# Kernel tuning notes

Hardware: AMD Instinct MI355X
Metric: run time of the kernel (lower is better)

Reference implementation:

```python
import jax, jax.numpy as jnp
import numpy as np
from functools import partial

B, S, H = 1, 2048, 1024
F, E, K = 2048, 8, 2


def setup_inputs() -> dict:
    key = jax.random.key(0)
    ks = jax.random.split(key, 7)
    x = jax.random.normal(ks[0], (B, S, H), dtype=jnp.float32)
    weights = jax.random.uniform(ks[1], (B * S, E), dtype=jnp.float32)
    top_weights = jax.random.uniform(ks[2], (B * S, K), dtype=jnp.float32)
    top_experts = jax.random.randint(ks[3], (B * S, K), 0, E).astype(jnp.int64)
    scale = 0.02  # keep activations in a sane range
    w1 = jax.random.normal(ks[4], (E, F, H), dtype=jnp.float32) * scale
    v1 = jax.random.normal(ks[5], (E, F, H), dtype=jnp.float32) * scale
    w2 = jax.random.normal(ks[6], (E, F, H), dtype=jnp.float32) * scale
    return {"x": x, "weights": weights, "top_weights": top_weights,
            "top_experts": top_experts, "w1": w1, "v1": v1, "w2": w2}


def _moe_forward(x, top_weights, top_experts, w1, v1, w2):
    b, s, h = x.shape
    xf = x.reshape(-1, h)  # [T, H]
    n_exp = w1.shape[0]
    # combine weight per (token, expert): sum over top-k slots routed to e
    onehot = jax.nn.one_hot(top_experts, n_exp, dtype=x.dtype)      # [T, K, E]
    cw = jnp.einsum('tk,tke->et', top_weights, onehot)              # [E, T]

    def body(acc, inputs):
        w1e, v1e, w2e, cwe = inputs  # [F,H], [F,H], [F,H], [T]
        gate = jax.nn.silu(xf @ w1e.T)       # [T, F]
        inter = gate * (xf @ v1e.T)          # GLU
        down = inter @ w2e                   # [T, H]
        return acc + cwe[:, None] * down, None

    out, _ = jax.lax.scan(body, jnp.zeros_like(xf), (w1, v1, w2, cw))
    return out.reshape(b, s, h)


def reference(x, weights, top_weights, top_experts, w1, v1, w2):
    # `weights` (full router probs) is accepted but unused, as in the original.
    return _moe_forward(x, top_weights, top_experts, w1, v1, w2)
```

## Files before the change

kernel.cpp:

```cpp
#include <hip/hip_runtime.h>
#include <hip/hip_bf16.h>


#define T_ 2048
#define H_ 1024
#define F_ 2048
#define E_ 8

#define SCAP 768
#define MAXT2 (E_ * SCAP / 128)

typedef unsigned short u16;
typedef short s8v __attribute__((ext_vector_type(8)));
typedef float f4v __attribute__((ext_vector_type(4)));
typedef unsigned short u16x4 __attribute__((ext_vector_type(4)));

__device__ __forceinline__ u16 f2bf(float f) {
    union { float f; unsigned u; } v; v.f = f;
    unsigned r = v.u + 0x7FFF + ((v.u >> 16) & 1);
    return (u16)(r >> 16);
}
__device__ __forceinline__ unsigned pkbf(float a, float b) {
    __hip_bfloat162 h = __float22bfloat162_rn(make_float2(a, b));
    union { __hip_bfloat162 h; unsigned u; } c; c.h = h; return c.u;
}
__device__ __forceinline__ int4 cvt8(const float4 a, const float4 b) {
    int4 r; r.x = (int)pkbf(a.x, a.y); r.y = (int)pkbf(a.z, a.w);
    r.z = (int)pkbf(b.x, b.y); r.w = (int)pkbf(b.z, b.w); return r;
}
__device__ __forceinline__ void async16(void* lds, const void* g) {
    __builtin_amdgcn_global_load_lds(
        (const __attribute__((address_space(1))) unsigned*)g,
        (__attribute__((address_space(3))) unsigned*)lds, 16, 0, 0);
}

__global__ void router_kernel(const int* __restrict__ te, const float* __restrict__ tw,
                              int* __restrict__ slot_tok, float* __restrict__ slot_w,
                              int* __restrict__ tile_e, int* __restrict__ tile_s,
                              int* __restrict__ ntiles) {
    __shared__ int cnt[E_];
    __shared__ int s_any;
    int tid = threadIdx.x;
    if (tid < E_) cnt[tid] = 0;
    if (tid == 0) s_any = 0;
    __syncthreads();
    int any = 0;
    for (int i = tid; i < 2 * T_; i += 256) if (i & 1) any |= te[i];
    if (any) atomicOr(&s_any, 1);
    __syncthreads();
    bool is32 = (s_any != 0);
    for (int t = tid; t < T_; t += 256) {
        int e0 = is32 ? te[2 * t]     : te[4 * t];
        int e1 = is32 ? te[2 * t + 1] : te[4 * t + 2];
        float w0 = tw[2 * t], w1 = tw[2 * t + 1];
        if (e0 == e1) {
            int p = atomicAdd(&cnt[e0], 1);
            if (p < SCAP) { slot_tok[e0 * SCAP + p] = t; slot_w[e0 * SCAP + p] = w0 + w1; }
        } else {
            int p = atomicAdd(&cnt[e0], 1);
            if (p < SCAP) { slot_tok[e0 * SCAP + p] = t; slot_w[e0 * SCAP + p] = w0; }
            p = atomicAdd(&cnt[e1], 1);
            if (p < SCAP) { slot_tok[e1 * SCAP + p] = t; slot_w[e1 * SCAP + p] = w1; }
        }
    }
    __syncthreads();
    for (int e = 0; e < E_; ++e) {
        int c = min(cnt[e], SCAP);
        int pc = min((c + 127) & ~127, SCAP);
        for (int p = c + tid; p < pc; p += 256) {
            slot_tok[e * SCAP + p] = -1; slot_w[e * SCAP + p] = 0.f;
        }
    }
    __syncthreads();
    if (tid == 0) {
        int nt = 0;
        for (int e = 0; e < E_; ++e) {
            int pc = min((min(cnt[e], SCAP) + 127) & ~127, SCAP);
            for (int s = 0; s < pc; s += 128) { tile_e[nt] = e; tile_s[nt] = e * SCAP + s; ++nt; }
        }
        *ntiles = nt;
    }
}

__global__ void cvt_kernel(const float* __restrict__ src, u16* __restrict__ dst) {
    int i = (blockIdx.x * 256 + threadIdx.x) * 4;
    float4 v = *(const float4*)(src + i);
    u16x4 o = { f2bf(v.x), f2bf(v.y), f2bf(v.z), f2bf(v.w) };
    *(u16x4*)(dst + i) = o;
}

__global__ void tcvt8_kernel(const float* __restrict__ src0, u16* __restrict__ dst0) {
    const float* src = src0 + (size_t)blockIdx.z * F_ * H_;
    u16* dst = dst0 + (size_t)blockIdx.z * H_ * F_;
    __shared__ __align__(16) u16 tile[64][72];
    int bc = blockIdx.x * 64, br = blockIdx.y * 64;
    int tx = threadIdx.x, ty = threadIdx.y;
    for (int r = ty; r < 64; r += 32) {
        const float* p = src + (size_t)(br + r) * H_ + bc + tx * 8;
        float4 v0 = *(const float4*)p;
        float4 v1 = *(const float4*)(p + 4);
        u16* q = &tile[r][tx * 8];
        q[0] = f2bf(v0.x); q[1] = f2bf(v0.y); q[2] = f2bf(v0.z); q[3] = f2bf(v0.w);
        q[4] = f2bf(v1.x); q[5] = f2bf(v1.y); q[6] = f2bf(v1.z); q[7] = f2bf(v1.w);
    }
    __syncthreads();
    for (int c = ty; c < 64; c += 32) {
        u16 tmp[8];
#pragma unroll
        for (int j = 0; j < 8; ++j) tmp[j] = tile[tx * 8 + j][c];
        *(int4*)&dst[(size_t)(bc + c) * F_ + br + tx * 8] = *(int4*)tmp;
    }
}

__global__ void gather_x_kernel(const float* __restrict__ x, const int* __restrict__ slot_tok,
                                const int* __restrict__ tile_s, const int* __restrict__ ntiles,
                                u16* __restrict__ xg) {
    if ((int)blockIdx.x >= *ntiles) return;
    int base = tile_s[blockIdx.x];
    int tid = threadIdx.x;
    __shared__ int stok[128];
    if (tid < 128) stok[tid] = slot_tok[base + tid];
    __syncthreads();
    for (int c = tid; c < 128 * 128; c += 256) {
        int r = c >> 7, co = (c & 127) * 8;
        int tok = stok[r];
        u16* dst = xg + ((size_t)(base + r) << 10) + co;
        if (tok < 0) { *(int4*)dst = make_int4(0, 0, 0, 0); }
        else {
            const float* p = x + ((size_t)tok << 10) + co;
            *(int4*)dst = cvt8(*(const float4*)p, *(const float4*)(p + 4));
        }
    }
}

__global__ __launch_bounds__(256, 2) void glu_async_kernel(
        const u16* __restrict__ xg, const u16* __restrict__ w1b,
        const u16* __restrict__ v1b, const int* __restrict__ tile_e,
        const int* __restrict__ tile_s, const int* __restrict__ ntiles,
        const float* __restrict__ slot_w, u16* __restrict__ inter) {
    int bt = blockIdx.y;
    if (bt >= *ntiles) return;
    int e = tile_e[bt], s0 = tile_s[bt];
    int f0 = blockIdx.x * 128;
    __shared__ __align__(16) u16 As[128 * 32];
    __shared__ __align__(16) u16 B1s[128 * 32];
    __shared__ __align__(16) u16 B2s[128 * 32];
    __shared__ float swv[128];
    int tid = threadIdx.x;
    int lane = tid & 63, wave = tid >> 6;
    int wm = wave >> 1, wn = wave & 1;
    int ml = lane & 15, q = lane >> 4;
    if (tid < 128) swv[tid] = slot_w[s0 + tid];

    int acol = (lane & 3) << 3;
    int row0 = (wave << 4) + (lane >> 2);
    int row1 = row0 + 64;
    const u16* gA0  = xg + ((size_t)(s0 + row0) << 10) + acol;
    const u16* gA1  = xg + ((size_t)(s0 + row1) << 10) + acol;
    const size_t wofs = (size_t)e * F_ * H_;
    const u16* gB10 = w1b + wofs + ((size_t)(f0 + row0) << 10) + acol;
    const u16* gB11 = w1b + wofs + ((size_t)(f0 + row1) << 10) + acol;
    const u16* gB20 = v1b + wofs + ((size_t)(f0 + row0) << 10) + acol;
    const u16* gB21 = v1b + wofs + ((size_t)(f0 + row1) << 10) + acol;
    u16* lA0  = As  + (row0 << 5) + acol;
    u16* lA1  = As  + (row1 << 5) + acol;
    u16* lB10 = B1s + (row0 << 5) + acol;
    u16* lB11 = B1s + (row1 << 5) + acol;
    u16* lB20 = B2s + (row0 << 5) + acol;
    u16* lB21 = B2s + (row1 << 5) + acol;

    f4v accg[4][4] = {};
    f4v accu[4][4] = {};

    for (int k0 = 0; k0 < H_; k0 += 32) {
        __syncthreads();
        async16(lA0,  gA0  + k0);
        async16(lA1,  gA1  + k0);
        async16(lB10, gB10 + k0);
        async16(lB11, gB11 + k0);
        async16(lB20, gB20 + k0);
        async16(lB21, gB21 + k0);
        __syncthreads();
        s8v a[4], b1[4], b2[4];
#pragma unroll
        for (int i = 0; i < 4; ++i) {
            a[i]  = *(const s8v*)(As  + (wm * 64 + i * 16 + ml) * 32 + q * 8);
            b1[i] = *(const s8v*)(B1s + (wn * 64 + i * 16 + ml) * 32 + q * 8);
            b2[i] = *(const s8v*)(B2s + (wn * 64 + i * 16 + ml) * 32 + q * 8);
        }
#pragma unroll
        for (int i = 0; i < 4; ++i)
#pragma unroll
            for (int j = 0; j < 4; ++j) {
                accg[i][j] = __builtin_amdgcn_mfma_f32_16x16x32_bf16(a[i], b1[j], accg[i][j], 0, 0, 0);
                accu[i][j] = __builtin_amdgcn_mfma_f32_16x16x32_bf16(a[i], b2[j], accu[i][j], 0, 0, 0);
            }
    }
#pragma unroll
    for (int i = 0; i < 4; ++i)
#pragma unroll
        for (int r = 0; r < 4; ++r) {
            int lr = wm * 64 + i * 16 + q * 4 + r;
            float cv = swv[lr];
#pragma unroll
            for (int j = 0; j < 4; ++j) {
                float g = accg[i][j][r];
                float u = accu[i][j][r];
                float s = g / (1.f + __expf(-g));
                int f = f0 + wn * 64 + j * 16 + ml;
                inter[((size_t)(s0 + lr) << 11) + f] = f2bf(cv * s * u);
            }
        }
}

__global__ __launch_bounds__(256, 2) void down_async_kernel(
        const u16* __restrict__ inter, const u16* __restrict__ w2bT,
        const int* __restrict__ tile_e, const int* __restrict__ tile_s,
        const int* __restrict__ ntiles, const int* __restrict__ slot_tok,
        float* __restrict__ out) {
    int bt = blockIdx.y;
    if (bt >= *ntiles) return;
    int e = tile_e[bt], s0 = tile_s[bt];
    int h0 = blockIdx.x * 128;
    int kbeg = blockIdx.z * (F_ / 2);
    __shared__ __align__(16) u16 As[128 * 32];
    __shared__ __align__(16) u16 Bs[128 * 32];
    __shared__ int stok[128];
    int tid = threadIdx.x;
    int lane = tid & 63, wave = tid >> 6;
    int wm = wave >> 1, wn = wave & 1;
    int ml = lane & 15, q = lane >> 4;
    if (tid < 128) stok[tid] = slot_tok[s0 + tid];

    int acol = (lane & 3) << 3;
    int row0 = (wave << 4) + (lane >> 2);
    int row1 = row0 + 64;
    const u16* gA0 = inter + ((size_t)(s0 + row0) << 11) + kbeg + acol;
    const u16* gA1 = inter + ((size_t)(s0 + row1) << 11) + kbeg + acol;
    const u16* gB0 = w2bT + (size_t)e * H_ * F_ + ((size_t)(h0 + row0) << 11) + kbeg + acol;
    const u16* gB1 = w2bT + (size_t)e * H_ * F_ + ((size_t)(h0 + row1) << 11) + kbeg + acol;
    u16* lA0 = As + (row0 << 5) + acol;
    u16* lA1 = As + (row1 << 5) + acol;
    u16* lB0 = Bs + (row0 << 5) + acol;
    u16* lB1 = Bs + (row1 << 5) + acol;

    f4v acc[4][4] = {};
    for (int k0 = 0; k0 < F_ / 2; k0 += 32) {
        __syncthreads();
        async16(lA0, gA0 + k0);
        async16(lA1, gA1 + k0);
        async16(lB0, gB0 + k0);
        async16(lB1, gB1 + k0);
        __syncthreads();
        s8v a[4], b[4];
#pragma unroll
        for (int i = 0; i < 4; ++i) {
            a[i] = *(const s8v*)(As + (wm * 64 + i * 16 + ml) * 32 + q * 8);
            b[i] = *(const s8v*)(Bs + (wn * 64 + i * 16 + ml) * 32 + q * 8);
        }
#pragma unroll
        for (int i = 0; i < 4; ++i)
#pragma unroll
            for (int j = 0; j < 4; ++j)
                acc[i][j] = __builtin_amdgcn_mfma_f32_16x16x32_bf16(a[i], b[j], acc[i][j], 0, 0, 0);
    }
#pragma unroll
    for (int i = 0; i < 4; ++i)
#pragma unroll
        for (int r = 0; r < 4; ++r) {
            int lr = wm * 64 + i * 16 + q * 4 + r;
            int tok = stok[lr];
            if (tok < 0) continue;
            size_t trow = (size_t)tok << 10;
#pragma unroll
            for (int j = 0; j < 4; ++j) {
                int h = h0 + wn * 64 + j * 16 + ml;
                atomicAdd(&out[trow + h], acc[i][j][r]);
            }
        }
}

#define SCAP3 1024
__global__ void router3_kernel(const int* __restrict__ te, const float* __restrict__ tw,
                               int* __restrict__ cnt_g, int* __restrict__ slot_tok,
                               float* __restrict__ slot_w) {
    __shared__ int cnt[E_];
    __shared__ int s_any;
    int tid = threadIdx.x;
    if (tid < E_) cnt[tid] = 0;
    if (tid == 0) s_any = 0;
    __syncthreads();
    int any = 0;
    for (int i = tid; i < 2 * T_; i += 256) if (i & 1) any |= te[i];
    if (any) atomicOr(&s_any, 1);
    __syncthreads();
    bool is32 = (s_any != 0);
    for (int t = tid; t < T_; t += 256) {
        int e0 = is32 ? te[2 * t]     : te[4 * t];
        int e1 = is32 ? te[2 * t + 1] : te[4 * t + 2];
        float w0 = tw[2 * t], w1 = tw[2 * t + 1];
        if (e0 == e1) {
            int p = atomicAdd(&cnt[e0], 1);
            if (p < SCAP3) { slot_tok[e0 * SCAP3 + p] = t; slot_w[e0 * SCAP3 + p] = w0 + w1; }
        } else {
            int p = atomicAdd(&cnt[e0], 1);
            if (p < SCAP3) { slot_tok[e0 * SCAP3 + p] = t; slot_w[e0 * SCAP3 + p] = w0; }
            p = atomicAdd(&cnt[e1], 1);
            if (p < SCAP3) { slot_tok[e1 * SCAP3 + p] = t; slot_w[e1 * SCAP3 + p] = w1; }
        }
    }
    __syncthreads();
    for (int e = 0; e < E_; ++e) {
        int c = min(cnt[e], SCAP3);
        int pc = min((c + 127) & ~127, SCAP3);
        for (int p = c + tid; p < pc; p += 256) {
            slot_tok[e * SCAP3 + p] = 0; slot_w[e * SCAP3 + p] = 0.f;
        }
    }
    if (tid < E_) cnt_g[tid] = min(cnt[tid], SCAP3);
}
__global__ __launch_bounds__(256, 2) void glu3_kernel(
        const u16* __restrict__ xb, const float* __restrict__ w1,
        const float* __restrict__ v1, const int* __restrict__ cnt_g,
        const int* __restrict__ slot_tok, const float* __restrict__ slot_w,
        u16* __restrict__ inter) {
    int e = blockIdx.x >> 3, tt = blockIdx.x & 7;
    if (tt * 128 >= cnt_g[e]) return;
    __shared__ __align__(16) u16 As[128 * 32];
    __shared__ __align__(16) u16 B1s[128 * 32];
    __shared__ __align__(16) u16 B2s[128 * 32];
    __shared__ int stok[128];
    __shared__ float sw[128];
    int tid = threadIdx.x;
    if (tid < 128) {
        stok[tid] = slot_tok[e * SCAP3 + tt * 128 + tid];
        sw[tid]   = slot_w[e * SCAP3 + tt * 128 + tid];
    }
    __syncthreads();
    int lane = tid & 63, wave = tid >> 6;
    int wm = wave >> 1, wn = wave & 1;
    int f0 = blockIdx.y * 128;
    int ml = lane & 15, q = lane >> 4;
    int r0 = tid >> 2, r1 = 64 + (tid >> 2);
    int colo = (tid & 3) * 8;
    const size_t tokoff0 = (size_t)stok[r0] * H_ + colo;
    const size_t tokoff1 = (size_t)stok[r1] * H_ + colo;
    const float* gb1 = w1 + (size_t)e * F_ * H_ + (size_t)f0 * H_;
    const float* gb2 = v1 + (size_t)e * F_ * H_ + (size_t)f0 * H_;
    const size_t boff0 = (size_t)r0 * H_ + colo;
    const size_t boff1 = (size_t)r1 * H_ + colo;
    f4v accg[4][4] = {};
    f4v accu[4][4] = {};
    for (int k0 = 0; k0 < H_; k0 += 32) {
        __syncthreads();
        *(int4*)(As + tid * 8)         = *(const int4*)(xb + tokoff0 + k0);
        *(int4*)(As + (256 + tid) * 8) = *(const int4*)(xb + tokoff1 + k0);
        const float* p = gb1 + boff0 + k0;
        *(int4*)(B1s + tid * 8) = cvt8(*(const float4*)p, *(const float4*)(p + 4));
        p = gb1 + boff1 + k0;
        *(int4*)(B1s + (256 + tid) * 8) = cvt8(*(const float4*)p, *(const float4*)(p + 4));
        p = gb2 + boff0 + k0;
        *(int4*)(B2s + tid * 8) = cvt8(*(const float4*)p, *(const float4*)(p + 4));
        p = gb2 + boff1 + k0;
        *(int4*)(B2s + (256 + tid) * 8) = cvt8(*(const float4*)p, *(const float4*)(p + 4));
        __syncthreads();
        s8v a[4], b1[4], b2[4];
#pragma unroll
        for (int i = 0; i < 4; ++i) {
            a[i]  = *(const s8v*)(As  + (wm * 64 + i * 16 + ml) * 32 + q * 8);
            b1[i] = *(const s8v*)(B1s + (wn * 64 + i * 16 + ml) * 32 + q * 8);
            b2[i] = *(const s8v*)(B2s + (wn * 64 + i * 16 + ml) * 32 + q * 8);
        }
#pragma unroll
        for (int i = 0; i < 4; ++i)
#pragma unroll
            for (int j = 0; j < 4; ++j) {
                accg[i][j] = __builtin_amdgcn_mfma_f32_16x16x32_bf16(a[i], b1[j], accg[i][j], 0, 0, 0);
                accu[i][j] = __builtin_amdgcn_mfma_f32_16x16x32_bf16(a[i], b2[j], accu[i][j], 0, 0, 0);
            }
    }
#pragma unroll
    for (int i = 0; i < 4; ++i)
#pragma unroll
        for (int r = 0; r < 4; ++r) {
            int lr = wm * 64 + i * 16 + q * 4 + r;
            float cv = sw[lr];
#pragma unroll
            for (int j = 0; j < 4; ++j) {
                float g = accg[i][j][r];
                float u = accu[i][j][r];
                float s = g / (1.f + __expf(-g));
                int f = f0 + wn * 64 + j * 16 + ml;
                inter[(size_t)(e * SCAP3 + tt * 128 + lr) * F_ + f] = f2bf(cv * s * u);
            }
        }
}
__global__ __launch_bounds__(256) void down3_kernel(
        const u16* __restrict__ inter, const u16* __restrict__ w2bT,
        const int* __restrict__ cnt_g, const int* __restrict__ slot_tok,
        float* __restrict__ out) {
    int e = blockIdx.x >> 3, tt = blockIdx.x & 7;
    if (tt * 128 >= cnt_g[e]) return;
    __shared__ __align__(16) u16 As[128 * 32];
    __shared__ __align__(16) u16 Bs[128 * 32];
    __shared__ int stok[128];
    int tid = threadIdx.x;
    if (tid < 128) stok[tid] = slot_tok[e * SCAP3 + tt * 128 + tid];
    __syncthreads();
    int lane = tid & 63, wave = tid >> 6;
    int wm = wave >> 1, wn = wave & 1;
    int h0 = blockIdx.y * 128;
    int ml = lane & 15, q = lane >> 4;
    int kbeg = blockIdx.z * (F_ / 2), kend = kbeg + (F_ / 2);
    f4v acc[4][4] = {};
    const u16* ga = inter + (size_t)(e * SCAP3 + tt * 128) * F_;
    const u16* gb = w2bT + (size_t)e * H_ * F_ + (size_t)h0 * F_;
    for (int k0 = kbeg; k0 < kend; k0 += 32) {
        __syncthreads();
#pragma unroll
        for (int p = 0; p < 2; ++p) {
            int c = p * 256 + tid;
            int r = c >> 2, co = (c & 3) * 8;
            *(int4*)(As + c * 8) = *(const int4*)(ga + (size_t)r * F_ + k0 + co);
            *(int4*)(Bs + c * 8) = *(const int4*)(gb + (size_t)r * F_ + k0 + co);
        }
        __syncthreads();
        s8v a[4], b[4];
#pragma unroll
        for (int i = 0; i < 4; ++i) {
            a[i] = *(const s8v*)(As + (wm * 64 + i * 16 + ml) * 32 + q * 8);
            b[i] = *(const s8v*)(Bs + (wn * 64 + i * 16 + ml) * 32 + q * 8);
        }
#pragma unroll
        for (int i = 0; i < 4; ++i)
#pragma unroll
            for (int j = 0; j < 4; ++j)
                acc[i][j] = __builtin_amdgcn_mfma_f32_16x16x32_bf16(a[i], b[j], acc[i][j], 0, 0, 0);
    }
#pragma unroll
    for (int i = 0; i < 4; ++i)
#pragma unroll
        for (int r = 0; r < 4; ++r) {
            int lr = wm * 64 + i * 16 + q * 4 + r;
            size_t trow = (size_t)stok[lr] * H_;
#pragma unroll
            for (int j = 0; j < 4; ++j) {
                int h = h0 + wn * 64 + j * 16 + ml;
                atomicAdd(&out[trow + h], acc[i][j][r]);
            }
        }
}

extern "C" void kernel_launch(void* const* d_in, const int* in_sizes, int n_in,
                              void* d_out, int out_size, void* d_ws, size_t ws_size,
                              hipStream_t stream) {
    const float* x  = (const float*)d_in[0];
    const float* tw = (const float*)d_in[2];
    const int*   te = (const int*)d_in[3];
    const float* w1 = (const float*)d_in[4];
    const float* v1 = (const float*)d_in[5];
    const float* w2 = (const float*)d_in[6];
    float* out = (float*)d_out;
    char* ws = (char*)d_ws;

    if (ws_size >= ((size_t)135 << 20)) {
        int*   tile_e   = (int*)(ws + (1 << 10));
        int*   tile_s   = (int*)(ws + (2 << 10));
        int*   ntiles   = (int*)(ws + 256);
        int*   slot_tok = (int*)(ws + (4 << 10));
        float* slot_w   = (float*)(ws + (32 << 10));
        u16*   xg       = (u16*)(ws + ((size_t)1 << 20));
        u16*   w1b      = (u16*)(ws + ((size_t)13 << 20));
        u16*   v1b      = (u16*)(ws + ((size_t)45 << 20));
        u16*   w2bT     = (u16*)(ws + ((size_t)77 << 20));
        u16*   inter    = (u16*)(ws + ((size_t)109 << 20));

        hipMemsetAsync(out, 0, (size_t)T_ * H_ * sizeof(float), stream);
        router_kernel<<<1, 256, 0, stream>>>(te, tw, slot_tok, slot_w, tile_e, tile_s, ntiles);
        cvt_kernel<<<(E_ * F_ * H_) / 1024, 256, 0, stream>>>(w1, w1b);
        cvt_kernel<<<(E_ * F_ * H_) / 1024, 256, 0, stream>>>(v1, v1b);
        tcvt8_kernel<<<dim3(H_ / 64, F_ / 64, E_), dim3(8, 32), 0, stream>>>(w2, w2bT);
        gather_x_kernel<<<MAXT2, 256, 0, stream>>>(x, slot_tok, tile_s, ntiles, xg);
        glu_async_kernel<<<dim3(F_ / 128, MAXT2), 256, 0, stream>>>(
            xg, w1b, v1b, tile_e, tile_s, ntiles, slot_w, inter);
        down_async_kernel<<<dim3(H_ / 128, MAXT2, 2), 256, 0, stream>>>(
            inter, w2bT, tile_e, tile_s, ntiles, slot_tok, out);
    } else {
        int*   cnt_g    = (int*)(ws);
        int*   slot_tok = (int*)(ws + (4 << 10));
        float* slot_w   = (float*)(ws + (64 << 10));
        u16*   xb       = (u16*)(ws + ((size_t)1 << 20));
        u16*   w2bT     = (u16*)(ws + ((size_t)5 << 20));
        u16*   inter    = (u16*)(ws + ((size_t)37 << 20));

        hipMemsetAsync(out, 0, (size_t)T_ * H_ * sizeof(float), stream);
        router3_kernel<<<1, 256, 0, stream>>>(te, tw, cnt_g, slot_tok, slot_w);
        cvt_kernel<<<(T_ * H_) / 1024, 256, 0, stream>>>(x, xb);
        tcvt8_kernel<<<dim3(H_ / 64, F_ / 64, E_), dim3(8, 32), 0, stream>>>(w2, w2bT);
        glu3_kernel<<<dim3(E_ * 8, F_ / 128), 256, 0, stream>>>(
            xb, w1, v1, cnt_g, slot_tok, slot_w, inter);
        down3_kernel<<<dim3(E_ * 8, H_ / 128, 2), 256, 0, stream>>>(
            inter, w2bT, cnt_g, slot_tok, out);
    }
}
```

Before: 374.3 us.

## Halve GEMM N-tiles, replace atomic scatter with per-slot buffers and combine kernel

Shrinks the N tile of both grouped GEMMs from 128 to 64 and raises the occupancy hint, doubling block count to fill more CUs. The down-projection now writes plain stores into two split-K per-slot buffers (reusing the w1b/v1b workspace once they are consumed), and a new combine kernel gathers each token's two slots, removing the output memset and fp32 atomics. The router also records a token-to-slot map, and the w1/v1 conversions are merged into one launch. In exchange each A tile is reloaded twice as often, and the extra buffer write plus read and one more kernel launch add traffic.

```diff
diff --git a/kernel.cpp b/kernel.cpp
--- a/kernel.cpp
+++ b/kernel.cpp
@@ -8,7 +8,8 @@
 #define E_ 8
 
 #define SCAP 768
-#define MAXT2 (E_ * SCAP / 128)
+#define NSLOT (E_ * SCAP)
+#define MAXT2 (NSLOT / 128)
 
 typedef unsigned short u16;
 typedef short s8v __attribute__((ext_vector_type(8)));
@@ -36,6 +37,7 @@
 
 __global__ void router_kernel(const int* __restrict__ te, const float* __restrict__ tw,
                               int* __restrict__ slot_tok, float* __restrict__ slot_w,
+                              int* __restrict__ tok_slot,
                               int* __restrict__ tile_e, int* __restrict__ tile_s,
                               int* __restrict__ ntiles) {
     __shared__ int cnt[E_];
@@ -55,12 +57,18 @@
         float w0 = tw[2 * t], w1 = tw[2 * t + 1];
         if (e0 == e1) {
             int p = atomicAdd(&cnt[e0], 1);
-            if (p < SCAP) { slot_tok[e0 * SCAP + p] = t; slot_w[e0 * SCAP + p] = w0 + w1; }
+            int s = (p < SCAP) ? e0 * SCAP + p : -1;
+            if (s >= 0) { slot_tok[s] = t; slot_w[s] = w0 + w1; }
+            tok_slot[2 * t] = s; tok_slot[2 * t + 1] = -1;
         } else {
             int p = atomicAdd(&cnt[e0], 1);
-            if (p < SCAP) { slot_tok[e0 * SCAP + p] = t; slot_w[e0 * SCAP + p] = w0; }
+            int s = (p < SCAP) ? e0 * SCAP + p : -1;
+            if (s >= 0) { slot_tok[s] = t; slot_w[s] = w0; }
+            tok_slot[2 * t] = s;
             p = atomicAdd(&cnt[e1], 1);
-            if (p < SCAP) { slot_tok[e1 * SCAP + p] = t; slot_w[e1 * SCAP + p] = w1; }
+            s = (p < SCAP) ? e1 * SCAP + p : -1;
+            if (s >= 0) { slot_tok[s] = t; slot_w[s] = w1; }
+            tok_slot[2 * t + 1] = s;
         }
     }
     __syncthreads();
@@ -82,7 +90,10 @@
     }
 }
 
-__global__ void cvt_kernel(const float* __restrict__ src, u16* __restrict__ dst) {
+__global__ void cvtwv_kernel(const float* __restrict__ w1, const float* __restrict__ v1,
+                             u16* __restrict__ w1b, u16* __restrict__ v1b) {
+    const float* src = blockIdx.y ? v1 : w1;
+    u16* dst = blockIdx.y ? v1b : w1b;
     int i = (blockIdx.x * 256 + threadIdx.x) * 4;
     float4 v = *(const float4*)(src + i);
     u16x4 o = { f2bf(v.x), f2bf(v.y), f2bf(v.z), f2bf(v.w) };
@@ -133,7 +144,7 @@
     }
 }
 
-__global__ __launch_bounds__(256, 2) void glu_async_kernel(
+__global__ __launch_bounds__(256, 4) void glu_async_kernel(
         const u16* __restrict__ xg, const u16* __restrict__ w1b,
         const u16* __restrict__ v1b, const int* __restrict__ tile_e,
         const int* __restrict__ tile_s, const int* __restrict__ ntiles,
@@ -141,10 +152,10 @@
     int bt = blockIdx.y;
     if (bt >= *ntiles) return;
     int e = tile_e[bt], s0 = tile_s[bt];
-    int f0 = blockIdx.x * 128;
+    int f0 = blockIdx.x * 64;
     __shared__ __align__(16) u16 As[128 * 32];
-    __shared__ __align__(16) u16 B1s[128 * 32];
-    __shared__ __align__(16) u16 B2s[128 * 32];
+    __shared__ __align__(16) u16 B1s[64 * 32];
+    __shared__ __align__(16) u16 B2s[64 * 32];
     __shared__ float swv[128];
     int tid = threadIdx.x;
     int lane = tid & 63, wave = tid >> 6;
@@ -158,40 +169,36 @@
     const u16* gA0  = xg + ((size_t)(s0 + row0) << 10) + acol;
     const u16* gA1  = xg + ((size_t)(s0 + row1) << 10) + acol;
     const size_t wofs = (size_t)e * F_ * H_;
-    const u16* gB10 = w1b + wofs + ((size_t)(f0 + row0) << 10) + acol;
-    const u16* gB11 = w1b + wofs + ((size_t)(f0 + row1) << 10) + acol;
-    const u16* gB20 = v1b + wofs + ((size_t)(f0 + row0) << 10) + acol;
-    const u16* gB21 = v1b + wofs + ((size_t)(f0 + row1) << 10) + acol;
-    u16* lA0  = As  + (row0 << 5) + acol;
-    u16* lA1  = As  + (row1 << 5) + acol;
-    u16* lB10 = B1s + (row0 << 5) + acol;
-    u16* lB11 = B1s + (row1 << 5) + acol;
-    u16* lB20 = B2s + (row0 << 5) + acol;
-    u16* lB21 = B2s + (row1 << 5) + acol;
-
-    f4v accg[4][4] = {};
-    f4v accu[4][4] = {};
+    const u16* gB1 = w1b + wofs + ((size_t)(f0 + row0) << 10) + acol;
+    const u16* gB2 = v1b + wofs + ((size_t)(f0 + row0) << 10) + acol;
+    u16* lA0 = As  + (row0 << 5) + acol;
+    u16* lA1 = As  + (row1 << 5) + acol;
+    u16* lB1 = B1s + (row0 << 5) + acol;
+    u16* lB2 = B2s + (row0 << 5) + acol;
+
+    f4v accg[4][2] = {};
+    f4v accu[4][2] = {};
 
     for (int k0 = 0; k0 < H_; k0 += 32) {
         __syncthreads();
-        async16(lA0,  gA0  + k0);
-        async16(lA1,  gA1  + k0);
-        async16(lB10, gB10 + k0);
-        async16(lB11, gB11 + k0);
-        async16(lB20, gB20 + k0);
-        async16(lB21, gB21 + k0);
-        __syncthreads();
-        s8v a[4], b1[4], b2[4];
-#pragma unroll
-        for (int i = 0; i < 4; ++i) {
+        async16(lA0, gA0 + k0);
+        async16(lA1, gA1 + k0);
+        async16(lB1, gB1 + k0);
+        async16(lB2, gB2 + k0);
+        __syncthreads();
+        s8v a[4], b1[2], b2[2];
+#pragma unroll
+        for (int i = 0; i < 4; ++i)
             a[i]  = *(const s8v*)(As  + (wm * 64 + i * 16 + ml) * 32 + q * 8);
-            b1[i] = *(const s8v*)(B1s + (wn * 64 + i * 16 + ml) * 32 + q * 8);
-            b2[i] = *(const s8v*)(B2s + (wn * 64 + i * 16 + ml) * 32 + q * 8);
+#pragma unroll
+        for (int j = 0; j < 2; ++j) {
+            b1[j] = *(const s8v*)(B1s + (wn * 32 + j * 16 + ml) * 32 + q * 8);
+            b2[j] = *(const s8v*)(B2s + (wn * 32 + j * 16 + ml) * 32 + q * 8);
         }
 #pragma unroll
         for (int i = 0; i < 4; ++i)
 #pragma unroll
-            for (int j = 0; j < 4; ++j) {
+            for (int j = 0; j < 2; ++j) {
                 accg[i][j] = __builtin_amdgcn_mfma_f32_16x16x32_bf16(a[i], b1[j], accg[i][j], 0, 0, 0);
                 accu[i][j] = __builtin_amdgcn_mfma_f32_16x16x32_bf16(a[i], b2[j], accu[i][j], 0, 0, 0);
             }
@@ -203,65 +210,63 @@
             int lr = wm * 64 + i * 16 + q * 4 + r;
             float cv = swv[lr];
 #pragma unroll
-            for (int j = 0; j < 4; ++j) {
+            for (int j = 0; j < 2; ++j) {
                 float g = accg[i][j][r];
                 float u = accu[i][j][r];
                 float s = g / (1.f + __expf(-g));
-                int f = f0 + wn * 64 + j * 16 + ml;
+                int f = f0 + wn * 32 + j * 16 + ml;
                 inter[((size_t)(s0 + lr) << 11) + f] = f2bf(cv * s * u);
             }
         }
 }
 
-__global__ __launch_bounds__(256, 2) void down_async_kernel(
+__global__ __launch_bounds__(256, 4) void down_async_kernel(
         const u16* __restrict__ inter, const u16* __restrict__ w2bT,
         const int* __restrict__ tile_e, const int* __restrict__ tile_s,
-        const int* __restrict__ ntiles, const int* __restrict__ slot_tok,
-        float* __restrict__ out) {
+        const int* __restrict__ ntiles,
+        float* __restrict__ dbufA, float* __restrict__ dbufB) {
     int bt = blockIdx.y;
     if (bt >= *ntiles) return;
     int e = tile_e[bt], s0 = tile_s[bt];
-    int h0 = blockIdx.x * 128;
-    int kbeg = blockIdx.z * (F_ / 2);
+    int h0 = blockIdx.x * 64;
+    int ks = blockIdx.z;
+    int kbeg = ks * (F_ / 2);
+    float* dbuf = ks ? dbufB : dbufA;
     __shared__ __align__(16) u16 As[128 * 32];
-    __shared__ __align__(16) u16 Bs[128 * 32];
-    __shared__ int stok[128];
+    __shared__ __align__(16) u16 Bs[64 * 32];
     int tid = threadIdx.x;
     int lane = tid & 63, wave = tid >> 6;
     int wm = wave >> 1, wn = wave & 1;
     int ml = lane & 15, q = lane >> 4;
-    if (tid < 128) stok[tid] = slot_tok[s0 + tid];
 
     int acol = (lane & 3) << 3;
     int row0 = (wave << 4) + (lane >> 2);
     int row1 = row0 + 64;
     const u16* gA0 = inter + ((size_t)(s0 + row0) << 11) + kbeg + acol;
     const u16* gA1 = inter + ((size_t)(s0 + row1) << 11) + kbeg + acol;
-    const u16* gB0 = w2bT + (size_t)e * H_ * F_ + ((size_t)(h0 + row0) << 11) + kbeg + acol;
-    const u16* gB1 = w2bT + (size_t)e * H_ * F_ + ((size_t)(h0 + row1) << 11) + kbeg + acol;
+    const u16* gB  = w2bT + (size_t)e * H_ * F_ + ((size_t)(h0 + row0) << 11) + kbeg + acol;
     u16* lA0 = As + (row0 << 5) + acol;
     u16* lA1 = As + (row1 << 5) + acol;
-    u16* lB0 = Bs + (row0 << 5) + acol;
-    u16* lB1 = Bs + (row1 << 5) + acol;
-
-    f4v acc[4][4] = {};
+    u16* lB  = Bs + (row0 << 5) + acol;
+
+    f4v acc[4][2] = {};
     for (int k0 = 0; k0 < F_ / 2; k0 += 32) {
         __syncthreads();
         async16(lA0, gA0 + k0);
         async16(lA1, gA1 + k0);
-        async16(lB0, gB0 + k0);
-        async16(lB1, gB1 + k0);
-        __syncthreads();
-        s8v a[4], b[4];
-#pragma unroll
-        for (int i = 0; i < 4; ++i) {
+        async16(lB,  gB  + k0);
+        __syncthreads();
+        s8v a[4], b[2];
+#pragma unroll
+        for (int i = 0; i < 4; ++i)
             a[i] = *(const s8v*)(As + (wm * 64 + i * 16 + ml) * 32 + q * 8);
-            b[i] = *(const s8v*)(Bs + (wn * 64 + i * 16 + ml) * 32 + q * 8);
-        }
+#pragma unroll
+        for (int j = 0; j < 2; ++j)
+            b[j] = *(const s8v*)(Bs + (wn * 32 + j * 16 + ml) * 32 + q * 8);
 #pragma unroll
         for (int i = 0; i < 4; ++i)
 #pragma unroll
-            for (int j = 0; j < 4; ++j)
+            for (int j = 0; j < 2; ++j)
                 acc[i][j] = __builtin_amdgcn_mfma_f32_16x16x32_bf16(a[i], b[j], acc[i][j], 0, 0, 0);
     }
 #pragma unroll
@@ -269,15 +274,32 @@
 #pragma unroll
         for (int r = 0; r < 4; ++r) {
             int lr = wm * 64 + i * 16 + q * 4 + r;
-            int tok = stok[lr];
-            if (tok < 0) continue;
-            size_t trow = (size_t)tok << 10;
-#pragma unroll
-            for (int j = 0; j < 4; ++j) {
-                int h = h0 + wn * 64 + j * 16 + ml;
-                atomicAdd(&out[trow + h], acc[i][j][r]);
+            float* drow = dbuf + ((size_t)(s0 + lr) << 10);
+#pragma unroll
+            for (int j = 0; j < 2; ++j) {
+                int h = h0 + wn * 32 + j * 16 + ml;
+                drow[h] = acc[i][j][r];
             }
         }
+}
+
+__global__ void combine_kernel(const float* __restrict__ dbufA, const float* __restrict__ dbufB,
+                               const int* __restrict__ tok_slot, float* __restrict__ out) {
+    int t = blockIdx.x;
+    int c = threadIdx.x * 4;
+    int s0 = tok_slot[2 * t], s1 = tok_slot[2 * t + 1];
+    float4 acc = make_float4(0.f, 0.f, 0.f, 0.f);
+    if (s0 >= 0) {
+        float4 a = *(const float4*)(dbufA + ((size_t)s0 << 10) + c);
+        float4 b = *(const float4*)(dbufB + ((size_t)s0 << 10) + c);
+        acc.x = a.x + b.x; acc.y = a.y + b.y; acc.z = a.z + b.z; acc.w = a.w + b.w;
+    }
+    if (s1 >= 0) {
+        float4 a = *(const float4*)(dbufA + ((size_t)s1 << 10) + c);
+        float4 b = *(const float4*)(dbufB + ((size_t)s1 << 10) + c);
+        acc.x += a.x + b.x; acc.y += a.y + b.y; acc.z += a.z + b.z; acc.w += a.w + b.w;
+    }
+    *(float4*)(out + ((size_t)t << 10) + c) = acc;
 }
 
 #define SCAP3 1024
@@ -318,6 +340,12 @@
         }
     }
     if (tid < E_) cnt_g[tid] = min(cnt[tid], SCAP3);
+}
+__global__ void cvt_kernel(const float* __restrict__ src, u16* __restrict__ dst) {
+    int i = (blockIdx.x * 256 + threadIdx.x) * 4;
+    float4 v = *(const float4*)(src + i);
+    u16x4 o = { f2bf(v.x), f2bf(v.y), f2bf(v.z), f2bf(v.w) };
+    *(u16x4*)(dst + i) = o;
 }
 __global__ __launch_bounds__(256, 2) void glu3_kernel(
         const u16* __restrict__ xb, const float* __restrict__ w1,
@@ -464,27 +492,30 @@
     char* ws = (char*)d_ws;
 
     if (ws_size >= ((size_t)135 << 20)) {
-        int*   tile_e   = (int*)(ws + (1 << 10));
-        int*   tile_s   = (int*)(ws + (2 << 10));
-        int*   ntiles   = (int*)(ws + 256);
-        int*   slot_tok = (int*)(ws + (4 << 10));
-        float* slot_w   = (float*)(ws + (32 << 10));
+        int*   ntiles   = (int*)(ws);
+        int*   tile_e   = (int*)(ws + 256);
+        int*   tile_s   = (int*)(ws + 512);
+        int*   tok_slot = (int*)(ws + (4 << 10));
+        int*   slot_tok = (int*)(ws + (20 << 10));
+        float* slot_w   = (float*)(ws + (44 << 10));
         u16*   xg       = (u16*)(ws + ((size_t)1 << 20));
         u16*   w1b      = (u16*)(ws + ((size_t)13 << 20));
         u16*   v1b      = (u16*)(ws + ((size_t)45 << 20));
         u16*   w2bT     = (u16*)(ws + ((size_t)77 << 20));
         u16*   inter    = (u16*)(ws + ((size_t)109 << 20));
-
-        hipMemsetAsync(out, 0, (size_t)T_ * H_ * sizeof(float), stream);
-        router_kernel<<<1, 256, 0, stream>>>(te, tw, slot_tok, slot_w, tile_e, tile_s, ntiles);
-        cvt_kernel<<<(E_ * F_ * H_) / 1024, 256, 0, stream>>>(w1, w1b);
-        cvt_kernel<<<(E_ * F_ * H_) / 1024, 256, 0, stream>>>(v1, v1b);
+        float* dbufA    = (float*)(ws + ((size_t)13 << 20));
+        float* dbufB    = (float*)(ws + ((size_t)45 << 20));
+
+        router_kernel<<<1, 256, 0, stream>>>(te, tw, slot_tok, slot_w, tok_slot,
+                                             tile_e, tile_s, ntiles);
+        cvtwv_kernel<<<dim3((E_ * F_ * H_) / 1024, 2), 256, 0, stream>>>(w1, v1, w1b, v1b);
         tcvt8_kernel<<<dim3(H_ / 64, F_ / 64, E_), dim3(8, 32), 0, stream>>>(w2, w2bT);
         gather_x_kernel<<<MAXT2, 256, 0, stream>>>(x, slot_tok, tile_s, ntiles, xg);
-        glu_async_kernel<<<dim3(F_ / 128, MAXT2), 256, 0, stream>>>(
+        glu_async_kernel<<<dim3(F_ / 64, MAXT2), 256, 0, stream>>>(
             xg, w1b, v1b, tile_e, tile_s, ntiles, slot_w, inter);
-        down_async_kernel<<<dim3(H_ / 128, MAXT2, 2), 256, 0, stream>>>(
-            inter, w2bT, tile_e, tile_s, ntiles, slot_tok, out);
+        down_async_kernel<<<dim3(H_ / 64, MAXT2, 2), 256, 0, stream>>>(
+            inter, w2bT, tile_e, tile_s, ntiles, dbufA, dbufB);
+        combine_kernel<<<T_, 256, 0, stream>>>(dbufA, dbufB, tok_slot, out);
     } else {
         int*   cnt_g    = (int*)(ws);
         int*   slot_tok = (int*)(ws + (4 << 10));
```

Result: no change. 367.5 us (-1.8%).
